# Kernel optimization log

Measured on AMD Instinct MI355X. Metric: run time of the kernel, lower is better.

The kernel has to match this reference:

```python
import jax, jax.numpy as jnp
import numpy as np

TAU = 0.01
WEIGHT = 1.0
N = 4096


def _isotonic_nondecreasing(y):
    """L2 isotonic regression: argmin_{v_1<=...<=v_n} ||v-y||^2, via the
    min-max formula v_i = max_{j<=i} min_{k>=i} mean(y[j..k]). O(n^2) but fully
    vectorized; the vjp reproduces the block-averaging Jacobian of PAV."""
    n = y.shape[0]
    cs = jnp.concatenate([jnp.zeros((1,), y.dtype), jnp.cumsum(y)])
    j = jnp.arange(n)[:, None]
    k = jnp.arange(n)[None, :]
    M = (cs[k + 1] - cs[j]) / (k - j + 1).astype(y.dtype)  # mean(y[j..k]) for j<=k
    big = jnp.asarray(jnp.inf, y.dtype)
    M = jnp.where(j <= k, M, big)
    # S[j,i] = min_{k>=i} M[j,k]  (reverse cummin along k)
    S = jax.lax.cummin(M[:, ::-1], axis=1)[:, ::-1]
    S = jnp.where(j <= k, S, -big)  # invalidate j>i before cummax over j
    T = jax.lax.cummax(S, axis=0)   # T[i,i] = max_{j<=i} S[j,i]
    return jnp.diagonal(T)


def _soft_rank(values, reg):
    """Differentiable ascending ranks via L2 projection onto the permutahedron
    of w=[n,...,1] (Blondel et al. / torchsort soft_rank, l2 regularization)."""
    n = values.shape[0]
    s_scaled = values / reg
    perm = jnp.argsort(-s_scaled)            # descending order
    s = s_scaled[perm]
    w = jnp.arange(n, 0, -1, dtype=values.dtype)
    v = -_isotonic_nondecreasing(-(s - w))
    primal = s - v
    inv = jnp.argsort(perm)
    return primal[inv]


def _soft_perm(x, tau):
    """Row-stochastic soft permutation: P[i,j] = softmax_j(-(sort(x)_i - x_j)^2/tau).
    As tau->0, P@y reorders y by ascending x."""
    xs = jnp.sort(x)
    logits = -((xs[:, None] - x[None, :]) ** 2) / tau  # [n, n]
    return jax.nn.softmax(logits, axis=-1)


def setup_inputs() -> dict:
    key = jax.random.key(0)
    k1, k2 = jax.random.split(key)
    preds = jax.random.normal(k1, (N,), dtype=jnp.float32)
    target = jax.random.normal(k2, (N,), dtype=jnp.float32)
    return {"preds": preds, "target": target}


def reference(preds, target):
    n = preds.shape[0]
    P = _soft_perm(preds, TAU)               # [n, n]
    y_sorted = P @ target                    # target soft-reordered by preds
    r_sorted = _soft_rank(y_sorted, TAU)     # soft ranks of reordered target
    diff_sum = jnp.abs(r_sorted[1:] - r_sorted[:-1]).sum()
    xi_soft = 1.0 - 3.0 * diff_sum / (n * n - 1)
    loss = -WEIGHT * xi_soft
    return loss, jax.lax.stop_gradient(xi_soft)
```

## Files before the change

### kernel.cpp

```cpp
#include <hip/hip_runtime.h>
#include <hip/hip_bf16.h>
#include <math.h>

#define N 4096


__global__ __launch_bounds__(512, 4)
void k_A(const float* __restrict__ preds, const float* __restrict__ target,
         float* __restrict__ y) {
    __shared__ __align__(16) float4 sp4[N / 4];
    __shared__ __align__(16) float4 st4[N / 4];
    int tid = threadIdx.x;
    int b = blockIdx.x;
    int lane = tid & 63, wid = tid >> 6;
    const float4* gp = (const float4*)preds;
    const float4* gt = (const float4*)target;
    sp4[tid] = gp[tid];
    sp4[tid + 512] = gp[tid + 512];
    st4[tid] = gt[tid];
    st4[tid + 512] = gt[tid + 512];
    __syncthreads();
    const float* sp = (const float*)sp4;
    int i0 = b * 8 + wid;
    float xv = sp[i0];
    float Z = 0.f, Nm = 0.f;
    int cnt = 0;
    #pragma unroll 4
    for (int m = 0; m < 16; m++) {
        int q = lane + 64 * m;
        float4 p4 = sp4[q];
        float4 t4 = st4[q];
        int j = q * 4;
        float d0 = xv - p4.x, d1 = xv - p4.y, d2 = xv - p4.z, d3 = xv - p4.w;
        float e0 = __expf(-100.0f * d0 * d0);
        float e1 = __expf(-100.0f * d1 * d1);
        float e2 = __expf(-100.0f * d2 * d2);
        float e3 = __expf(-100.0f * d3 * d3);
        Z += (e0 + e1) + (e2 + e3);
        Nm += e0 * t4.x + e1 * t4.y + e2 * t4.z + e3 * t4.w;
        cnt += (p4.x < xv) || (p4.x == xv && (j + 0) < i0);
        cnt += (p4.y < xv) || (p4.y == xv && (j + 1) < i0);
        cnt += (p4.z < xv) || (p4.z == xv && (j + 2) < i0);
        cnt += (p4.w < xv) || (p4.w == xv && (j + 3) < i0);
    }
    #pragma unroll
    for (int d = 32; d; d >>= 1) {
        Z += __shfl_down(Z, d);
        Nm += __shfl_down(Nm, d);
        cnt += __shfl_down(cnt, d);
    }
    if (lane == 0) y[cnt] = Nm / Z;
}

__global__ __launch_bounds__(1024, 4)
void k_B(const float* __restrict__ y, float* __restrict__ s_out,
         int* __restrict__ perm_out) {
    __shared__ __align__(16) float sy[N];
    __shared__ int part[16][65];
    int tid = threadIdx.x;
    int b = blockIdx.x;
    ((float4*)sy)[tid] = ((const float4*)y)[tid];
    __syncthreads();
    int eloc = tid & 15;
    int slice = tid >> 4;
    int i = b * 16 + eloc;
    float v = sy[i];
    int cnt = 0;
    const float4* sy4 = (const float4*)sy;
    #pragma unroll
    for (int it = 0; it < 16; it++) {
        int q = slice * 16 + ((it + slice) & 15);
        float4 a = sy4[q];
        int j = q * 4;
        cnt += (a.x > v) || (a.x == v && (j + 0) < i);
        cnt += (a.y > v) || (a.y == v && (j + 1) < i);
        cnt += (a.z > v) || (a.z == v && (j + 2) < i);
        cnt += (a.w > v) || (a.w == v && (j + 3) < i);
    }
    part[eloc][slice] = cnt;
    __syncthreads();
    if (tid < 16) {
        int r = 0;
        #pragma unroll
        for (int q = 0; q < 64; q++) r += part[tid][q];
        int i2 = b * 16 + tid;
        s_out[r] = sy[i2] * 100.0f;
        perm_out[r] = i2;
    }
}

__global__ __launch_bounds__(512, 2)
void k_C(const float* __restrict__ s, float* __restrict__ P) {
    __shared__ float mT[4][8][68];
    __shared__ float iT[4][8][68];
    __shared__ double cj[16];
    __shared__ double wsum[8];
    int tid = threadIdx.x;
    int b = blockIdx.x;
    int j0 = b * 16;
    int kbase = tid * 8;
    int lane = tid & 63, wid = tid >> 6;
    int ce = tid & 7, ct = tid >> 3;
    double loc[8];
    {
        const float4* s4 = (const float4*)s;
        double tot = 0.0;
        #pragma unroll
        for (int q = 0; q < 2; q++) {
            float4 a = s4[tid * 2 + q];
            int t0 = kbase + q * 4;
            tot += (double)(N - (t0 + 0)) - (double)a.x; loc[q * 4 + 0] = tot;
            tot += (double)(N - (t0 + 1)) - (double)a.y; loc[q * 4 + 1] = tot;
            tot += (double)(N - (t0 + 2)) - (double)a.z; loc[q * 4 + 2] = tot;
            tot += (double)(N - (t0 + 3)) - (double)a.w; loc[q * 4 + 3] = tot;
        }
        double w = tot;
        #pragma unroll
        for (int d = 1; d < 64; d <<= 1) {
            double o = __shfl_up(w, d);
            if (lane >= d) w += o;
        }
        if (lane == 63) wsum[wid] = w;
        __syncthreads();
        double base = 0.0;
        #pragma unroll
        for (int q = 0; q < 8; q++) if (q < wid) base += wsum[q];
        double excl = base + (w - tot);
        #pragma unroll
        for (int e = 0; e < 8; e++) loc[e] += excl;
        if (tid == 2 * b) {
            cj[0] = excl;
            #pragma unroll
            for (int m = 1; m < 8; m++) cj[m] = loc[m - 1];
        }
        if (tid == 2 * b + 1) {
            cj[8] = excl;
            #pragma unroll
            for (int m = 1; m < 8; m++) cj[8 + m] = loc[m - 1];
        }
    }
    __syncthreads();
    float vloc[8];
    #pragma unroll
    for (int e = 0; e < 8; e++) vloc[e] = -INFINITY;
    float ls[4][8];
    bool live = (tid >= 2 * b);
    for (int grp = 0; grp < 4; grp++) {
        if (live) {
            #pragma unroll
            for (int rq = 0; rq < 4; rq++) {
                int j = j0 + grp * 4 + rq;
                double csj = cj[grp * 4 + rq];
                float run = INFINITY;
                #pragma unroll
                for (int e = 7; e >= 0; e--) {
                    int k = kbase + e;
                    float f = INFINITY;
                    if (k >= j) f = (float)(loc[e] - csj) * __builtin_amdgcn_rcpf((float)(k - j + 1));
                    run = fminf(f, run);
                    ls[rq][e] = run;
                }
                mT[rq][ce][ct] = run;
            }
        } else {
            #pragma unroll
            for (int rq = 0; rq < 4; rq++) mT[rq][ce][ct] = INFINITY;
        }
        __syncthreads();
        if (wid < 4) {
            float m0 = mT[wid][0][lane];
            float m1 = mT[wid][1][lane];
            float m2 = mT[wid][2][lane];
            float m3 = mT[wid][3][lane];
            float m4 = mT[wid][4][lane];
            float m5 = mT[wid][5][lane];
            float m6 = mT[wid][6][lane];
            float m7 = mT[wid][7][lane];
            float s7 = m7;
            float s6 = fminf(m6, s7);
            float s5 = fminf(m5, s6);
            float s4 = fminf(m4, s5);
            float s3 = fminf(m3, s4);
            float s2 = fminf(m2, s3);
            float s1 = fminf(m1, s2);
            float s0 = fminf(m0, s1);
            float t = s0;
            #pragma unroll
            for (int d = 1; d < 64; d <<= 1) {
                float o = __shfl_down(t, d);
                if (lane + d < 64) t = fminf(t, o);
            }
            float after = __shfl_down(t, 1);
            if (lane == 63) after = INFINITY;
            iT[wid][0][lane] = fminf(s0, after);
            iT[wid][1][lane] = fminf(s1, after);
            iT[wid][2][lane] = fminf(s2, after);
            iT[wid][3][lane] = fminf(s3, after);
            iT[wid][4][lane] = fminf(s4, after);
            iT[wid][5][lane] = fminf(s5, after);
            iT[wid][6][lane] = fminf(s6, after);
            iT[wid][7][lane] = fminf(s7, after);
            if (lane == 63) iT[wid][0][64] = INFINITY;
        }
        __syncthreads();
        if (live) {
            int nc = tid + 1;
            #pragma unroll
            for (int rq = 0; rq < 4; rq++) {
                int j = j0 + grp * 4 + rq;
                float aft = iT[rq][nc & 7][nc >> 3];
                #pragma unroll
                for (int e = 0; e < 8; e++) {
                    int i = kbase + e;
                    float sv = fminf(ls[rq][e], aft);
                    if (i >= j) vloc[e] = fmaxf(vloc[e], sv);
                }
            }
        }
        __syncthreads();
    }
    if (tid >= 2 * b) {
        float4* P4 = (float4*)(P + (size_t)b * N);
        P4[tid * 2 + 0] = make_float4(vloc[0], vloc[1], vloc[2], vloc[3]);
        P4[tid * 2 + 1] = make_float4(vloc[4], vloc[5], vloc[6], vloc[7]);
    }
}

__global__ __launch_bounds__(1024, 4)
void k_reduce(const float* __restrict__ P, const float* __restrict__ s,
              const int* __restrict__ perm, float* __restrict__ r) {
    __shared__ float part[16][65];
    int tid = threadIdx.x;
    int col = tid & 15;
    int slice = tid >> 4;
    int blk = blockIdx.x;
    int i = blk * 16 + col;
    float m = -INFINITY;
    #pragma unroll
    for (int q = 0; q < 4; q++) {
        int bb = slice * 4 + q;
        if (bb <= blk) m = fmaxf(m, P[(size_t)bb * N + i]);
    }
    part[col][slice] = m;
    __syncthreads();
    if (tid < 16) {
        float T = -INFINITY;
        #pragma unroll
        for (int q = 0; q < 64; q++) T = fmaxf(T, part[tid][q]);
        int i2 = blk * 16 + tid;
        r[perm[i2]] = s[i2] + T;
    }
}

__global__ __launch_bounds__(1024, 4)
void k_finish2(const float* __restrict__ r, float* __restrict__ out) {
    __shared__ double red[16];
    int tid = threadIdx.x;
    const float4* r4 = (const float4*)r;
    float4 x = r4[tid];
    float extra = (tid < 1023) ? r[tid * 4 + 4] : 0.0f;
    double acc = 0.0;
    acc += fabs((double)x.y - (double)x.x);
    acc += fabs((double)x.z - (double)x.y);
    acc += fabs((double)x.w - (double)x.z);
    if (tid < 1023) acc += fabs((double)extra - (double)x.w);
    #pragma unroll
    for (int dd = 32; dd; dd >>= 1) acc += __shfl_down(acc, dd);
    if ((tid & 63) == 0) red[tid >> 6] = acc;
    __syncthreads();
    if (tid == 0) {
        double ds = 0.0;
        #pragma unroll
        for (int q = 0; q < 16; q++) ds += red[q];
        double xi = 1.0 - 3.0 * ds / ((double)N * (double)N - 1.0);
        out[0] = (float)(-1.0 * xi);
        out[1] = (float)xi;
    }
}

extern "C" void kernel_launch(void* const* d_in, const int* in_sizes, int n_in,
                              void* d_out, int out_size, void* d_ws, size_t ws_size,
                              hipStream_t stream) {
    const float* preds  = (const float*)d_in[0];
    const float* target = (const float*)d_in[1];
    float* out = (float*)d_out;

    char* ws = (char*)d_ws;
    float* y    = (float*)(ws);
    float* s    = (float*)(ws + 16384);
    int*   perm = (int*)(ws + 32768);
    float* r    = (float*)(ws + 49152);
    float* P    = (float*)(ws + 81920);

    k_A<<<512, 512, 0, stream>>>(preds, target, y);
    k_B<<<256, 1024, 0, stream>>>(y, s, perm);
    k_C<<<256, 512, 0, stream>>>(s, P);
    k_reduce<<<256, 1024, 0, stream>>>(P, s, perm, r);
    k_finish2<<<1, 1024, 0, stream>>>(r, out);
}
```

Baseline: 86.07 us.

## Replace P matrix write and reduce kernel with atomicMax on order-encoded floats

Instead of writing a 256xN partial-max matrix and running a separate reduction kernel, k_C now folds its per-column maxima directly into a global int array with atomicMax, using an order-preserving float-to-int encoding. k_B initialises that array, and the final kernel applies the scatter by perm in shared memory before the abs-diff sum. This removes one kernel launch and about 4 MB of global write and read traffic. The cost is up to 256 contending atomics per element.

```diff
diff --git a/kernel.cpp b/kernel.cpp
--- a/kernel.cpp
+++ b/kernel.cpp
@@ -4,6 +4,14 @@
 
 #define N 4096
 
+
+__device__ __forceinline__ int f2o(float f) {
+    int i = __float_as_int(f);
+    return i < 0 ? (i ^ 0x7fffffff) : i;
+}
+__device__ __forceinline__ float o2f(int i) {
+    return __int_as_float(i < 0 ? (i ^ 0x7fffffff) : i);
+}
 
 __global__ __launch_bounds__(512, 4)
 void k_A(const float* __restrict__ preds, const float* __restrict__ target,
@@ -54,12 +62,13 @@
 
 __global__ __launch_bounds__(1024, 4)
 void k_B(const float* __restrict__ y, float* __restrict__ s_out,
-         int* __restrict__ perm_out) {
+         int* __restrict__ perm_out, int* __restrict__ Tenc) {
     __shared__ __align__(16) float sy[N];
     __shared__ int part[16][65];
     int tid = threadIdx.x;
     int b = blockIdx.x;
     ((float4*)sy)[tid] = ((const float4*)y)[tid];
+    if (tid < 16) Tenc[b * 16 + tid] = 0x80000000;
     __syncthreads();
     int eloc = tid & 15;
     int slice = tid >> 4;
@@ -90,7 +99,7 @@
 }
 
 __global__ __launch_bounds__(512, 2)
-void k_C(const float* __restrict__ s, float* __restrict__ P) {
+void k_C(const float* __restrict__ s, int* __restrict__ Tenc) {
     __shared__ float mT[4][8][68];
     __shared__ float iT[4][8][68];
     __shared__ double cj[16];
@@ -220,45 +229,29 @@
         __syncthreads();
     }
     if (tid >= 2 * b) {
-        float4* P4 = (float4*)(P + (size_t)b * N);
-        P4[tid * 2 + 0] = make_float4(vloc[0], vloc[1], vloc[2], vloc[3]);
-        P4[tid * 2 + 1] = make_float4(vloc[4], vloc[5], vloc[6], vloc[7]);
+        #pragma unroll
+        for (int e = 0; e < 8; e++) {
+            atomicMax(Tenc + kbase + e, f2o(vloc[e]));
+        }
     }
 }
 
 __global__ __launch_bounds__(1024, 4)
-void k_reduce(const float* __restrict__ P, const float* __restrict__ s,
-              const int* __restrict__ perm, float* __restrict__ r) {
-    __shared__ float part[16][65];
-    int tid = threadIdx.x;
-    int col = tid & 15;
-    int slice = tid >> 4;
-    int blk = blockIdx.x;
-    int i = blk * 16 + col;
-    float m = -INFINITY;
-    #pragma unroll
-    for (int q = 0; q < 4; q++) {
-        int bb = slice * 4 + q;
-        if (bb <= blk) m = fmaxf(m, P[(size_t)bb * N + i]);
-    }
-    part[col][slice] = m;
-    __syncthreads();
-    if (tid < 16) {
-        float T = -INFINITY;
-        #pragma unroll
-        for (int q = 0; q < 64; q++) T = fmaxf(T, part[tid][q]);
-        int i2 = blk * 16 + tid;
-        r[perm[i2]] = s[i2] + T;
-    }
-}
-
-__global__ __launch_bounds__(1024, 4)
-void k_finish2(const float* __restrict__ r, float* __restrict__ out) {
+void k_finish3(const int* __restrict__ Tenc, const float* __restrict__ s,
+               const int* __restrict__ perm, float* __restrict__ out) {
+    __shared__ __align__(16) float rl[N];
     __shared__ double red[16];
     int tid = threadIdx.x;
-    const float4* r4 = (const float4*)r;
-    float4 x = r4[tid];
-    float extra = (tid < 1023) ? r[tid * 4 + 4] : 0.0f;
+    int4 te = ((const int4*)Tenc)[tid];
+    float4 sv = ((const float4*)s)[tid];
+    int4 pe = ((const int4*)perm)[tid];
+    rl[pe.x] = sv.x + o2f(te.x);
+    rl[pe.y] = sv.y + o2f(te.y);
+    rl[pe.z] = sv.z + o2f(te.z);
+    rl[pe.w] = sv.w + o2f(te.w);
+    __syncthreads();
+    float4 x = ((const float4*)rl)[tid];
+    float extra = (tid < 1023) ? rl[tid * 4 + 4] : 0.0f;
     double acc = 0.0;
     acc += fabs((double)x.y - (double)x.x);
     acc += fabs((double)x.z - (double)x.y);
@@ -289,12 +282,10 @@
     float* y    = (float*)(ws);
     float* s    = (float*)(ws + 16384);
     int*   perm = (int*)(ws + 32768);
-    float* r    = (float*)(ws + 49152);
-    float* P    = (float*)(ws + 81920);
+    int*   Tenc = (int*)(ws + 49152);
 
     k_A<<<512, 512, 0, stream>>>(preds, target, y);
-    k_B<<<256, 1024, 0, stream>>>(y, s, perm);
-    k_C<<<256, 512, 0, stream>>>(s, P);
-    k_reduce<<<256, 1024, 0, stream>>>(P, s, perm, r);
-    k_finish2<<<1, 1024, 0, stream>>>(r, out);
-}
+    k_B<<<256, 1024, 0, stream>>>(y, s, perm, Tenc);
+    k_C<<<256, 512, 0, stream>>>(s, Tenc);
+    k_finish3<<<1, 1024, 0, stream>>>(Tenc, s, perm, out);
+}
```

Result: slower. 117.5 us (+36.6%).
